# Kernel tuning notes

Hardware: AMD Instinct MI355X
Metric: run time of the kernel (lower is better)

The kernel has to match this reference:

```python
import jax, jax.numpy as jnp
import numpy as np

N_USERS = 100_000
N_ITEMS = 100_000
D = 64
B = 16_384
L_U = 50   # items per user history
N_F = 32   # friends per user
L_I = 50   # users per item history


def setup_inputs() -> dict:
    key = jax.random.key(0)
    ks = jax.random.split(key, 22)
    s = 0.1  # xavier-ish scale for D=64
    return {
        "user_ids": jax.random.randint(ks[0], (B,), 0, N_USERS),
        "item_ids": jax.random.randint(ks[1], (B,), 0, N_ITEMS),
        "user_hist_items": jax.random.randint(ks[2], (B, L_U), 0, N_ITEMS),
        "user_hist_ratings": jax.random.uniform(ks[3], (B, L_U), jnp.float32, 1.0, 5.0),
        "user_friends": jax.random.randint(ks[4], (B, N_F), 0, N_USERS),
        "item_hist_users": jax.random.randint(ks[5], (B, L_I), 0, N_USERS),
        "item_hist_ratings": jax.random.uniform(ks[6], (B, L_I), jnp.float32, 1.0, 5.0),
        "embed_user": jax.random.normal(ks[7], (N_USERS, D), jnp.float32) * s,
        "embed_item": jax.random.normal(ks[8], (N_ITEMS, D), jnp.float32) * s,
        "W1": jax.random.normal(ks[9], (D, D), jnp.float32) * s,
        "W2": jax.random.normal(ks[10], (D, D), jnp.float32) * s,
        "W3": jax.random.normal(ks[11], (D, 1), jnp.float32) * s,
        "W4": jax.random.normal(ks[12], (D, D), jnp.float32) * s,
        "W5": jax.random.normal(ks[13], (D, D), jnp.float32) * s,
        "W6": jax.random.normal(ks[14], (D, 1), jnp.float32) * s,
        "W7": jax.random.normal(ks[15], (D, D), jnp.float32) * s,
        "W8": jax.random.normal(ks[16], (D, D), jnp.float32) * s,
        "W9": jax.random.normal(ks[17], (D, 1), jnp.float32) * s,
        "fc1_w": jax.random.normal(ks[18], (2 * D, D), jnp.float32) * s,
        "fc1_b": jnp.zeros((D,), jnp.float32),
        "fc2_w": jax.random.normal(ks[19], (D, 1), jnp.float32) * s,
        "fc2_b": jnp.zeros((1,), jnp.float32),
    }


def _attention(q_emb, neigh, Wq, Wk, Wa, ratings=None):
    # q_emb: [B, D]; neigh: [B, L, D]; ratings: [B, L] or None
    a = q_emb @ Wq  # [B, D]
    a = a[:, None, :] + neigh @ Wk  # [B, L, D]
    if ratings is not None:
        a = a + ratings[..., None] * neigh
    w = jax.nn.softmax((a @ Wa)[..., 0], axis=1)  # [B, L]
    return jnp.einsum("bl,bld->bd", w, neigh)


def reference(user_ids, item_ids, user_hist_items, user_hist_ratings,
              user_friends, item_hist_users, item_hist_ratings,
              embed_user, embed_item,
              W1, W2, W3, W4, W5, W6, W7, W8, W9,
              fc1_w, fc1_b, fc2_w, fc2_b):
    user_emb = embed_user[user_ids]          # [B, D]
    item_emb = embed_item[item_ids]          # [B, D]

    # user <- rated items attention (W1, W2, W3)
    hist_item_embs = embed_item[user_hist_items]        # [B, L_U, D]
    user_items_emb = _attention(user_emb, hist_item_embs, W1, W2, W3,
                                user_hist_ratings)

    # user <- friends attention (W4, W5, W6)
    friend_embs = embed_user[user_friends]               # [B, N_F, D]
    user_social_emb = _attention(user_emb, friend_embs, W4, W5, W6)

    user_emb_final = user_emb + user_items_emb + user_social_emb

    # item <- interacting users attention (W7, W8, W9)
    hist_user_embs = embed_user[item_hist_users]         # [B, L_I, D]
    item_users_emb = _attention(item_emb, hist_user_embs, W7, W8, W9,
                                item_hist_ratings)
    item_emb_final = item_emb + item_users_emb

    concat = jnp.concatenate([user_emb_final, item_emb_final], axis=1)  # [B, 2D]
    h = jax.nn.relu(concat @ fc1_w + fc1_b)
    out = (h @ fc2_w + fc2_b)[:, 0]  # [B]
    return out
```

## Files before the change

kernel.cpp:

```cpp
#include <hip/hip_runtime.h>
#include <hip/hip_bf16.h>
#include <math.h>

#define B_TOTAL 16384
#define D 64
#define L_U 50
#define N_F 32
#define L_I 50
#define ROWOFF(l) (((l) << 6) + ((((l) >> 2)) << 2))
#define TILE_FL 3248

__global__ void graphrec_setup(const float* __restrict__ W1, const float* __restrict__ W2,
                               const float* __restrict__ W3, const float* __restrict__ W4,
                               const float* __restrict__ W5, const float* __restrict__ W6,
                               const float* __restrict__ W7, const float* __restrict__ W8,
                               const float* __restrict__ W9, float* __restrict__ u) {
    int t = threadIdx.x;
    int w = t >> 6;
    int d = t & 63;
    const float* Wm;
    const float* Wv;
    switch (w) {
        case 0: Wm = W1; Wv = W3; break;
        case 1: Wm = W2; Wv = W3; break;
        case 2: Wm = W4; Wv = W6; break;
        case 3: Wm = W5; Wv = W6; break;
        case 4: Wm = W7; Wv = W9; break;
        default: Wm = W8; Wv = W9; break;
    }
    float s = 0.f;
    #pragma unroll
    for (int j = 0; j < D; ++j) s = fmaf(Wm[d * D + j], Wv[j], s);
    u[w * D + d] = s;
}

__device__ __forceinline__ float wred_sum(float x) {
    float t;
    #define STEP_ADD(ctrl, rmask)                                                        \
        t = __int_as_float(__builtin_amdgcn_update_dpp(0, __float_as_int(x),             \
                                                       ctrl, rmask, 0xf, false));        \
        x = x + t;
    STEP_ADD(0x111, 0xf)
    STEP_ADD(0x112, 0xf)
    STEP_ADD(0x114, 0xf)
    STEP_ADD(0x118, 0xf)
    STEP_ADD(0x142, 0xa)
    STEP_ADD(0x143, 0xc)
    #undef STEP_ADD
    return __int_as_float(__builtin_amdgcn_readlane(__float_as_int(x), 63));
}
__device__ __forceinline__ float wred_max(float x) {
    const int NEG_INF = 0xFF800000;
    float t;
    #define STEP_MAX(ctrl, rmask)                                                        \
        t = __int_as_float(__builtin_amdgcn_update_dpp(NEG_INF, __float_as_int(x),       \
                                                       ctrl, rmask, 0xf, false));        \
        x = fmaxf(x, t);
    STEP_MAX(0x111, 0xf)
    STEP_MAX(0x112, 0xf)
    STEP_MAX(0x114, 0xf)
    STEP_MAX(0x118, 0xf)
    STEP_MAX(0x142, 0xa)
    STEP_MAX(0x143, 0xc)
    #undef STEP_MAX
    return __int_as_float(__builtin_amdgcn_readlane(__float_as_int(x), 63));
}

template <int L>
__device__ __forceinline__ void stage_load(const float* __restrict__ table,
                                           int idxreg, int lane, float4* buf) {
    const int sub = lane >> 4;
    const int co = (lane & 15) << 2;
    #pragma unroll
    for (int g = 0; g < (L + 3) / 4; ++g) {
        int l = 4 * g + sub;
        if (l > L - 1) l = L - 1;
        int ridx = __builtin_amdgcn_ds_bpermute(l << 2, idxreg);
        buf[g] = *(const float4*)(table + (size_t)(unsigned)ridx * D + co);
    }
}

template <int L>
__device__ __forceinline__ void stage_write(const float4* buf, int lane, float* tile) {
    const int sub = lane >> 4;
    const int co = (lane & 15) << 2;
    #pragma unroll
    for (int g = 0; g < (L + 3) / 4; ++g) {
        int l = 4 * g + sub;
        if (l > L - 1) l = L - 1;
        *(float4*)(tile + (l << 6) + (g << 2) + co) = buf[g];
    }
}

template <int L, bool HAS_R>
__device__ __forceinline__ float attn_compute(float cq,
                                              const float4* __restrict__ u2g,
                                              const float4* __restrict__ wag,
                                              float r, int lane, const float* tile) {
    const int rl = (lane < L) ? lane : (L - 1);
    const float* row = tile + ROWOFF(rl);
    float dotU = 0.f, dotW = 0.f;
    #pragma unroll
    for (int j = 0; j < D / 4; ++j) {
        float4 n = *(const float4*)(row + 4 * j);
        float4 uu = u2g[j];
        dotU = fmaf(n.x, uu.x, fmaf(n.y, uu.y, fmaf(n.z, uu.z, fmaf(n.w, uu.w, dotU))));
        if (HAS_R) {
            float4 ww = wag[j];
            dotW = fmaf(n.x, ww.x, fmaf(n.y, ww.y, fmaf(n.z, ww.z, fmaf(n.w, ww.w, dotW))));
        }
    }
    float sc = cq + dotU;
    if (HAS_R) sc = fmaf(r, dotW, sc);
    sc = (lane < L) ? sc : -1e30f;

    float m = wred_max(sc);
    float e = __expf(sc - m);
    float s = wred_sum(e);
    float w = e * (1.0f / s);

    float acc = 0.f;
    #pragma unroll
    for (int l = 0; l < L; ++l) {
        float wl = __int_as_float(__builtin_amdgcn_readlane(__float_as_int(w), l));
        acc = fmaf(wl, tile[ROWOFF(l) + lane], acc);
    }
    return acc;
}

__global__ __launch_bounds__(256, 3) void graphrec_fwd(
        const int* __restrict__ user_ids, const int* __restrict__ item_ids,
        const int* __restrict__ uh_items, const float* __restrict__ uh_rat,
        const int* __restrict__ ufriends,
        const int* __restrict__ ih_users, const float* __restrict__ ih_rat,
        const float* __restrict__ eu, const float* __restrict__ ei,
        const float* __restrict__ W3, const float* __restrict__ W6,
        const float* __restrict__ W9,
        const float* __restrict__ fc1w, const float* __restrict__ fc1b,
        const float* __restrict__ fc2w, const float* __restrict__ fc2b,
        const float* __restrict__ u, float* __restrict__ out) {
    __shared__ __align__(16) float smem[4 * TILE_FL];
    const int lane = threadIdx.x & 63;
    const int wv = threadIdx.x >> 6;
    const int b = blockIdx.x * 4 + wv;
    float* tile = smem + wv * TILE_FL;

    int idxA = 0, idxB = 0, idxC = 0;
    float rA = 0.f, rC = 0.f;
    if (lane < L_U) {
        idxA = uh_items[b * L_U + lane];
        rA   = uh_rat[b * L_U + lane];
        idxC = ih_users[b * L_I + lane];
        rC   = ih_rat[b * L_I + lane];
    }
    if (lane < N_F) idxB = ufriends[b * N_F + lane];

    float4 bufA[(L_U + 3) / 4];
    float4 bufB[(N_F + 3) / 4];
    stage_load<L_U>(ei, idxA, lane, bufA);
    stage_load<N_F>(eu, idxB, lane, bufB);

    const int uid = user_ids[b];
    const int iid = item_ids[b];
    const float qu = eu[(size_t)uid * D + lane];
    const float qi = ei[(size_t)iid * D + lane];

    const float cqa = wred_sum(qu * u[lane]);
    const float cqb = wred_sum(qu * u[128 + lane]);
    const float cqc = wred_sum(qi * u[256 + lane]);

    stage_write<L_U>(bufA, lane, tile);
    float4 bufC[(L_I + 3) / 4];
    stage_load<L_I>(eu, idxC, lane, bufC);
    const float accA = attn_compute<L_U, true >(cqa, (const float4*)(u + 64),
                                                (const float4*)W3, rA, lane, tile);

    stage_write<N_F>(bufB, lane, tile);
    const float accB = attn_compute<N_F, false>(cqb, (const float4*)(u + 192),
                                                (const float4*)W6, 0.f, lane, tile);

    stage_write<L_I>(bufC, lane, tile);
    const float accC = attn_compute<L_I, true >(cqc, (const float4*)(u + 320),
                                                (const float4*)W9, rC, lane, tile);

    const float uf  = qu + accA + accB;
    const float itf = qi + accC;

    float h = fc1b[lane];
    #pragma unroll
    for (int k = 0; k < D; ++k) {
        float c = __int_as_float(__builtin_amdgcn_readlane(__float_as_int(uf), k));
        h = fmaf(c, fc1w[k * D + lane], h);
    }
    #pragma unroll
    for (int k = 0; k < D; ++k) {
        float c = __int_as_float(__builtin_amdgcn_readlane(__float_as_int(itf), k));
        h = fmaf(c, fc1w[(D + k) * D + lane], h);
    }
    h = fmaxf(h, 0.f);
    float o = wred_sum(h * fc2w[lane]);
    if (lane == 0) out[b] = o + fc2b[0];
}

extern "C" void kernel_launch(void* const* d_in, const int* in_sizes, int n_in,
                              void* d_out, int out_size, void* d_ws, size_t ws_size,
                              hipStream_t stream) {
    const int*   user_ids = (const int*)d_in[0];
    const int*   item_ids = (const int*)d_in[1];
    const int*   uh_items = (const int*)d_in[2];
    const float* uh_rat   = (const float*)d_in[3];
    const int*   ufriends = (const int*)d_in[4];
    const int*   ih_users = (const int*)d_in[5];
    const float* ih_rat   = (const float*)d_in[6];
    const float* eu       = (const float*)d_in[7];
    const float* ei       = (const float*)d_in[8];
    const float* W1 = (const float*)d_in[9];
    const float* W2 = (const float*)d_in[10];
    const float* W3 = (const float*)d_in[11];
    const float* W4 = (const float*)d_in[12];
    const float* W5 = (const float*)d_in[13];
    const float* W6 = (const float*)d_in[14];
    const float* W7 = (const float*)d_in[15];
    const float* W8 = (const float*)d_in[16];
    const float* W9 = (const float*)d_in[17];
    const float* fc1w = (const float*)d_in[18];
    const float* fc1b = (const float*)d_in[19];
    const float* fc2w = (const float*)d_in[20];
    const float* fc2b = (const float*)d_in[21];
    float* out = (float*)d_out;
    float* u   = (float*)d_ws;

    graphrec_setup<<<1, 384, 0, stream>>>(W1, W2, W3, W4, W5, W6, W7, W8, W9, u);
    graphrec_fwd<<<B_TOTAL / 4, 256, 0, stream>>>(
        user_ids, item_ids, uh_items, uh_rat, ufriends, ih_users, ih_rat,
        eu, ei, W3, W6, W9, fc1w, fc1b, fc2w, fc2b, u, out);
}
```

Before: 205.1 us.

## Keep gathered neighbor rows in registers instead of staging through LDS

Gathered neighbor embeddings now stay in registers: each lane holds 8 contiguous floats of one row, and rows are grouped eight per group. Score dot products come from segmented DPP reductions and the weighted sums are formed in registers, with only a small shared-memory partial buffer left for the cross-lane reduction. The per-wave LDS footprint drops from a full tile to under a thousand floats, and launch bounds rise to 4 blocks per CU. The fc1 loop also gets four independent accumulators. The cost is higher register pressure from holding up to 14 float4 buffers per lane, plus extra bpermute and LDS reduction traffic.

```diff
diff --git a/kernel.cpp b/kernel.cpp
--- a/kernel.cpp
+++ b/kernel.cpp
@@ -1,5 +1,4 @@
 #include <hip/hip_runtime.h>
-#include <hip/hip_bf16.h>
 #include <math.h>
 
 #define B_TOTAL 16384
@@ -7,8 +6,14 @@
 #define L_U 50
 #define N_F 32
 #define L_I 50
-#define ROWOFF(l) (((l) << 6) + ((((l) >> 2)) << 2))
-#define TILE_FL 3248
+
+#define PART_OFF 0
+#define SUA_OFF  520
+#define SWA_OFF  584
+#define SUB_OFF  648
+#define SUC_OFF  712
+#define SWC_OFF  776
+#define WAVE_FL  848
 
 __global__ void graphrec_setup(const float* __restrict__ W1, const float* __restrict__ W2,
                                const float* __restrict__ W3, const float* __restrict__ W4,
@@ -66,69 +71,98 @@
     return __int_as_float(__builtin_amdgcn_readlane(__float_as_int(x), 63));
 }
 
-template <int L>
-__device__ __forceinline__ void stage_load(const float* __restrict__ table,
-                                           int idxreg, int lane, float4* buf) {
-    const int sub = lane >> 4;
-    const int co = (lane & 15) << 2;
-    #pragma unroll
-    for (int g = 0; g < (L + 3) / 4; ++g) {
-        int l = 4 * g + sub;
-        if (l > L - 1) l = L - 1;
-        int ridx = __builtin_amdgcn_ds_bpermute(l << 2, idxreg);
-        buf[g] = *(const float4*)(table + (size_t)(unsigned)ridx * D + co);
-    }
-}
-
-template <int L>
-__device__ __forceinline__ void stage_write(const float4* buf, int lane, float* tile) {
-    const int sub = lane >> 4;
-    const int co = (lane & 15) << 2;
-    #pragma unroll
-    for (int g = 0; g < (L + 3) / 4; ++g) {
-        int l = 4 * g + sub;
-        if (l > L - 1) l = L - 1;
-        *(float4*)(tile + (l << 6) + (g << 2) + co) = buf[g];
-    }
-}
-
-template <int L, bool HAS_R>
-__device__ __forceinline__ float attn_compute(float cq,
-                                              const float4* __restrict__ u2g,
-                                              const float4* __restrict__ wag,
-                                              float r, int lane, const float* tile) {
-    const int rl = (lane < L) ? lane : (L - 1);
-    const float* row = tile + ROWOFF(rl);
-    float dotU = 0.f, dotW = 0.f;
-    #pragma unroll
-    for (int j = 0; j < D / 4; ++j) {
-        float4 n = *(const float4*)(row + 4 * j);
-        float4 uu = u2g[j];
-        dotU = fmaf(n.x, uu.x, fmaf(n.y, uu.y, fmaf(n.z, uu.z, fmaf(n.w, uu.w, dotU))));
+__device__ __forceinline__ float segred8(float x) {
+    float t;
+    t = __int_as_float(__builtin_amdgcn_update_dpp(0, __float_as_int(x), 0x111, 0xf, 0xf, false));
+    x = x + t;
+    t = __int_as_float(__builtin_amdgcn_update_dpp(0, __float_as_int(x), 0x112, 0xf, 0xf, false));
+    x = x + t;
+    t = __int_as_float(__builtin_amdgcn_update_dpp(0, __float_as_int(x), 0x114, 0xf, 0xf, false));
+    x = x + t;
+    return x;
+}
+
+template <int L, int NG>
+__device__ __forceinline__ void stage8(const float* __restrict__ table,
+                                       int idxreg, int sub, int co, float4* buf) {
+    #pragma unroll
+    for (int g = 0; g < NG; ++g) {
+        int r = 8 * g + sub;
+        if (r > L - 1) r = L - 1;
+        int ridx = __builtin_amdgcn_ds_bpermute(r << 2, idxreg);
+        const float* p = table + (unsigned)((ridx << 6) + co);
+        buf[2 * g]     = *(const float4*)(p);
+        buf[2 * g + 1] = *(const float4*)(p + 4);
+    }
+}
+
+template <int L, int NG, bool HAS_R>
+__device__ __forceinline__ float attn8(float cq, const float* __restrict__ u2,
+                                       const float* __restrict__ wa, float r,
+                                       int lane, int sub, int cc,
+                                       const float4* buf, float* __restrict__ su,
+                                       float* __restrict__ sw,
+                                       float* __restrict__ part) {
+    const float4 uu0 = ((const float4*)u2)[2 * cc];
+    const float4 uu1 = ((const float4*)u2)[2 * cc + 1];
+    float4 ww0 = {0.f, 0.f, 0.f, 0.f}, ww1 = {0.f, 0.f, 0.f, 0.f};
+    if (HAS_R) {
+        ww0 = ((const float4*)wa)[2 * cc];
+        ww1 = ((const float4*)wa)[2 * cc + 1];
+    }
+
+    #pragma unroll
+    for (int g = 0; g < NG; ++g) {
+        const float4 n0 = buf[2 * g];
+        const float4 n1 = buf[2 * g + 1];
+        float du = fmaf(n0.x, uu0.x, fmaf(n0.y, uu0.y, fmaf(n0.z, uu0.z,
+                   fmaf(n0.w, uu0.w, fmaf(n1.x, uu1.x, fmaf(n1.y, uu1.y,
+                   fmaf(n1.z, uu1.z, n1.w * uu1.w)))))));
+        du = segred8(du);
         if (HAS_R) {
-            float4 ww = wag[j];
-            dotW = fmaf(n.x, ww.x, fmaf(n.y, ww.y, fmaf(n.z, ww.z, fmaf(n.w, ww.w, dotW))));
+            float dw = fmaf(n0.x, ww0.x, fmaf(n0.y, ww0.y, fmaf(n0.z, ww0.z,
+                       fmaf(n0.w, ww0.w, fmaf(n1.x, ww1.x, fmaf(n1.y, ww1.y,
+                       fmaf(n1.z, ww1.z, n1.w * ww1.w)))))));
+            dw = segred8(dw);
+            if (cc == 7) { su[8 * g + sub] = du; sw[8 * g + sub] = dw; }
+        } else {
+            if (cc == 7) su[8 * g + sub] = du;
         }
     }
-    float sc = cq + dotU;
-    if (HAS_R) sc = fmaf(r, dotW, sc);
+
+    float sc = cq + su[lane];
+    if (HAS_R) sc = fmaf(r, sw[lane], sc);
     sc = (lane < L) ? sc : -1e30f;
-
-    float m = wred_max(sc);
-    float e = __expf(sc - m);
-    float s = wred_sum(e);
-    float w = e * (1.0f / s);
-
+    const float m = wred_max(sc);
+    const float e = __expf(sc - m);
+    const float s = wred_sum(e);
+    const float w = e * (1.0f / s);
+
+    float4 a0 = {0.f, 0.f, 0.f, 0.f}, a1 = {0.f, 0.f, 0.f, 0.f};
+    #pragma unroll
+    for (int g = 0; g < NG; ++g) {
+        const float wv = __int_as_float(
+            __builtin_amdgcn_ds_bpermute((8 * g + sub) << 2, __float_as_int(w)));
+        const float4 n0 = buf[2 * g];
+        const float4 n1 = buf[2 * g + 1];
+        a0.x = fmaf(wv, n0.x, a0.x); a0.y = fmaf(wv, n0.y, a0.y);
+        a0.z = fmaf(wv, n0.z, a0.z); a0.w = fmaf(wv, n0.w, a0.w);
+        a1.x = fmaf(wv, n1.x, a1.x); a1.y = fmaf(wv, n1.y, a1.y);
+        a1.z = fmaf(wv, n1.z, a1.z); a1.w = fmaf(wv, n1.w, a1.w);
+    }
+
+    const int s4 = lane & 4;
+    const int pw = lane << 3;
+    *(float4*)(part + pw + s4)       = a0;
+    *(float4*)(part + pw + (4 ^ s4)) = a1;
+    const int rb = (lane & 56) + ((lane & 7) ^ ((lane >> 3) & 4));
     float acc = 0.f;
     #pragma unroll
-    for (int l = 0; l < L; ++l) {
-        float wl = __int_as_float(__builtin_amdgcn_readlane(__float_as_int(w), l));
-        acc = fmaf(wl, tile[ROWOFF(l) + lane], acc);
-    }
+    for (int s2 = 0; s2 < 8; ++s2) acc += part[rb + 64 * s2];
     return acc;
 }
 
-__global__ __launch_bounds__(256, 3) void graphrec_fwd(
+__global__ __launch_bounds__(256, 4) void graphrec_fwd(
         const int* __restrict__ user_ids, const int* __restrict__ item_ids,
         const int* __restrict__ uh_items, const float* __restrict__ uh_rat,
         const int* __restrict__ ufriends,
@@ -139,11 +173,14 @@
         const float* __restrict__ fc1w, const float* __restrict__ fc1b,
         const float* __restrict__ fc2w, const float* __restrict__ fc2b,
         const float* __restrict__ u, float* __restrict__ out) {
-    __shared__ __align__(16) float smem[4 * TILE_FL];
+    __shared__ __align__(16) float smem[4 * WAVE_FL];
     const int lane = threadIdx.x & 63;
     const int wv = threadIdx.x >> 6;
     const int b = blockIdx.x * 4 + wv;
-    float* tile = smem + wv * TILE_FL;
+    float* ws = smem + wv * WAVE_FL;
+    const int sub = lane >> 3;
+    const int cc  = lane & 7;
+    const int co  = cc << 3;
 
     int idxA = 0, idxB = 0, idxC = 0;
     float rA = 0.f, rC = 0.f;
@@ -155,10 +192,10 @@
     }
     if (lane < N_F) idxB = ufriends[b * N_F + lane];
 
-    float4 bufA[(L_U + 3) / 4];
-    float4 bufB[(N_F + 3) / 4];
-    stage_load<L_U>(ei, idxA, lane, bufA);
-    stage_load<N_F>(eu, idxB, lane, bufB);
+    float4 bufA[14];
+    float4 bufB[8];
+    stage8<L_U, 7>(ei, idxA, sub, co, bufA);
+    stage8<N_F, 4>(eu, idxB, sub, co, bufB);
 
     const int uid = user_ids[b];
     const int iid = item_ids[b];
@@ -169,36 +206,47 @@
     const float cqb = wred_sum(qu * u[128 + lane]);
     const float cqc = wred_sum(qi * u[256 + lane]);
 
-    stage_write<L_U>(bufA, lane, tile);
-    float4 bufC[(L_I + 3) / 4];
-    stage_load<L_I>(eu, idxC, lane, bufC);
-    const float accA = attn_compute<L_U, true >(cqa, (const float4*)(u + 64),
-                                                (const float4*)W3, rA, lane, tile);
-
-    stage_write<N_F>(bufB, lane, tile);
-    const float accB = attn_compute<N_F, false>(cqb, (const float4*)(u + 192),
-                                                (const float4*)W6, 0.f, lane, tile);
-
-    stage_write<L_I>(bufC, lane, tile);
-    const float accC = attn_compute<L_I, true >(cqc, (const float4*)(u + 320),
-                                                (const float4*)W9, rC, lane, tile);
+    const float accA = attn8<L_U, 7, true >(cqa, u + 64, W3, rA, lane, sub, cc,
+                                            bufA, ws + SUA_OFF, ws + SWA_OFF,
+                                            ws + PART_OFF);
+    float4 bufC[14];
+    stage8<L_I, 7>(eu, idxC, sub, co, bufC);
+
+    const float accB = attn8<N_F, 4, false>(cqb, u + 192, W6, 0.f, lane, sub, cc,
+                                            bufB, ws + SUB_OFF, ws + SUB_OFF,
+                                            ws + PART_OFF);
+    const float accC = attn8<L_I, 7, true >(cqc, u + 320, W9, rC, lane, sub, cc,
+                                            bufC, ws + SUC_OFF, ws + SWC_OFF,
+                                            ws + PART_OFF);
 
     const float uf  = qu + accA + accB;
     const float itf = qi + accC;
 
-    float h = fc1b[lane];
-    #pragma unroll
-    for (int k = 0; k < D; ++k) {
-        float c = __int_as_float(__builtin_amdgcn_readlane(__float_as_int(uf), k));
-        h = fmaf(c, fc1w[k * D + lane], h);
-    }
-    #pragma unroll
-    for (int k = 0; k < D; ++k) {
-        float c = __int_as_float(__builtin_amdgcn_readlane(__float_as_int(itf), k));
-        h = fmaf(c, fc1w[(D + k) * D + lane], h);
-    }
-    h = fmaxf(h, 0.f);
-    float o = wred_sum(h * fc2w[lane]);
+    float h0 = fc1b[lane], h1 = 0.f, h2 = 0.f, h3 = 0.f;
+    #pragma unroll
+    for (int k = 0; k < D; k += 4) {
+        h0 = fmaf(__int_as_float(__builtin_amdgcn_readlane(__float_as_int(uf), k + 0)),
+                  fc1w[(k + 0) * D + lane], h0);
+        h1 = fmaf(__int_as_float(__builtin_amdgcn_readlane(__float_as_int(uf), k + 1)),
+                  fc1w[(k + 1) * D + lane], h1);
+        h2 = fmaf(__int_as_float(__builtin_amdgcn_readlane(__float_as_int(uf), k + 2)),
+                  fc1w[(k + 2) * D + lane], h2);
+        h3 = fmaf(__int_as_float(__builtin_amdgcn_readlane(__float_as_int(uf), k + 3)),
+                  fc1w[(k + 3) * D + lane], h3);
+    }
+    #pragma unroll
+    for (int k = 0; k < D; k += 4) {
+        h0 = fmaf(__int_as_float(__builtin_amdgcn_readlane(__float_as_int(itf), k + 0)),
+                  fc1w[(D + k + 0) * D + lane], h0);
+        h1 = fmaf(__int_as_float(__builtin_amdgcn_readlane(__float_as_int(itf), k + 1)),
+                  fc1w[(D + k + 1) * D + lane], h1);
+        h2 = fmaf(__int_as_float(__builtin_amdgcn_readlane(__float_as_int(itf), k + 2)),
+                  fc1w[(D + k + 2) * D + lane], h2);
+        h3 = fmaf(__int_as_float(__builtin_amdgcn_readlane(__float_as_int(itf), k + 3)),
+                  fc1w[(D + k + 3) * D + lane], h3);
+    }
+    const float h = fmaxf((h0 + h1) + (h2 + h3), 0.f);
+    const float o = wred_sum(h * fc2w[lane]);
     if (lane == 0) out[b] = o + fc2b[0];
 }
 
```

Measured after the change: 209.0 us. No clear change (+1.9%).
